# Performance work log

Hardware: AMD Instinct MI355X
Metric: run time of the kernel (lower is better)

The kernel has to match this reference:

```python
import jax, jax.numpy as jnp
import numpy as np

B = 1024
IN_H, IN_W = 128, 128
KH, KW = 10, 10
SH, SW = 5, 5
PH, PW = 2, 2
HP, WP = IN_H + 2 * PH, IN_W + 2 * PW          # padded dims: 132, 132
NKH = (IN_H - KH + 2 * PH) // SH + 1            # 25
NKW = (IN_W - KW + 2 * PW) // SW + 1            # 25
NK = NKH * NKW                                  # 625


def _build_weight_matrix(kernel_weights):
    """kernel_weights: [NK, KH, KW] -> sparse-structured dense [HP*WP, NK].
    Faithful to LocallyConnected2dV2._create_weight_matrix, vectorized."""
    i = jnp.arange(NK)
    start_i = (i // NKW) * SH                   # [NK]
    start_j = (i % NKW) * SW                    # [NK]
    # flat row index for each (kernel, k, l) tap in padded image
    rows = ((start_i[:, None, None] + jnp.arange(KH)[None, :, None]) * WP
            + start_j[:, None, None] + jnp.arange(KW)[None, None, :])  # [NK,KH,KW]
    rows = rows.reshape(NK, KH * KW)
    cols = i[:, None]                           # [NK,1] broadcasts over taps
    W = jnp.zeros((HP * WP, NK), dtype=kernel_weights.dtype)
    return W.at[rows, cols].set(kernel_weights.reshape(NK, KH * KW))


def setup_inputs() -> dict:
    key = jax.random.key(0)
    kx, kw, kb = jax.random.split(key, 3)
    x = jax.random.normal(kx, (B, IN_H, IN_W), dtype=jnp.float32)
    kernel_weights = jax.random.normal(kw, (NK, KH, KW), dtype=jnp.float32)
    W = _build_weight_matrix(kernel_weights)    # [HP*WP, NK]
    bias = jax.random.normal(kb, (NKH, NKW), dtype=jnp.float32)
    return {"x": x, "W": W, "bias": bias}


def reference(x, W, bias):
    # zero-pad spatial dims, flatten, dense GEMM against sparse-structured W
    xp = jnp.pad(x, ((0, 0), (PH, PH), (PW, PW)))          # [B,HP,WP]
    xf = xp.reshape(x.shape[0], HP * WP)                   # [B,HP*WP]
    out = xf @ W                                           # [B,NK]
    out = out.reshape(x.shape[0], NKH, NKW)
    return out + bias
```

## Files before the change

### kernel.cpp

```cpp
#include <hip/hip_runtime.h>

typedef _Float16 f16x2 __attribute__((ext_vector_type(2)));
typedef __fp16  fp16x2 __attribute__((ext_vector_type(2)));

constexpr int NKW  = 25, NK = 625;
constexpr int WPADR = 132;
constexpr int WPT   = 160;
constexpr int RST   = 35;
constexpr int IMG   = 8;
constexpr int NSLAB = 6;
constexpr int MAXR  = 30;

union U2H { unsigned int u; f16x2 h; fp16x2 p; };

__global__ void gather_wp(const float* __restrict__ W, _Float16* __restrict__ wgpT) {
    int t = blockIdx.x * 256 + threadIdx.x;
    if (t >= NK * WPT) return;
    int k = t / WPT, p = t % WPT;
    int di = p >> 4, s = p & 15;
    int ki = k / NKW, kj = k % NKW;
    int o = (5 * kj + 2) & 3;
    int j = s - o;
    float val = 0.f;
    if (j >= 0 && j < 10)
        val = W[(size_t)((ki * 5 + di) * WPADR + kj * 5 + j) * NK + k];
    wgpT[((size_t)(p >> 3) * NK + k) * 8 + (p & 7)] = (_Float16)val;
}

__device__ __forceinline__ float dot2acc(unsigned int a, unsigned int b, float c) {
    U2H ua, ub; ua.u = a; ub.u = b;
#if __has_builtin(__builtin_amdgcn_fdot2)
    return __builtin_amdgcn_fdot2(ua.h, ub.h, c, false);
#else
    return c + (float)ua.h.x * (float)ub.h.x + (float)ua.h.y * (float)ub.h.y;
#endif
}

template <bool USE_WG>
__global__ __launch_bounds__(256, 4)
void lc2d_pipe(const float* __restrict__ x, const _Float16* __restrict__ wgpT,
               const float* __restrict__ Wfull,
               const float* __restrict__ bias, float* __restrict__ out) {
    __shared__ uint2 xs[2][MAXR * RST];

    const int flat = blockIdx.x;
    const int xcd  = flat & 7;
    const int j_   = flat >> 3;
    const int grp  = xcd + 8 * (j_ & 15);
    const int slab = j_ >> 4;
    const int K0   = slab ? (4 * slab + 1) : 0;
    const int NKI  = slab ? 4 : 5;
    const int R    = 5 * NKI + 5;
    const int NOUT = NKI * NKW;
    const int row0 = 5 * K0 - 2;
    const int tid  = threadIdx.x;
    const int b0   = grp * IMG;

    const int lane = tid & 63;
    const int pairidx = (tid >> 6) * 32 + (lane & 31);
    const int half = (lane >> 5) & 1;
    const bool active = pairidx < NOUT;
    const int ki_l = pairidx / 25;
    const int kj   = pairidx - ki_l * 25;
    const int k    = (K0 + ki_l) * NKW + kj;
    const int di0  = half * 5;

    uint4 wq[10];
    float bval = 0.f;
    if (active) {
        if (USE_WG) {
            const uint4* wt4 = reinterpret_cast<const uint4*>(wgpT);
#pragma unroll
            for (int j = 0; j < 10; ++j) wq[j] = wt4[(size_t)(half * 10 + j) * NK + k];
        } else {
            const int o = (5 * kj + 2) & 3;
#pragma unroll
            for (int j = 0; j < 10; ++j) {
                const int di = di0 + (j >> 1), pb = (j & 1) * 8;
                unsigned int uu[4];
#pragma unroll
                for (int m = 0; m < 4; ++m) {
                    float f0 = 0.f, f1 = 0.f;
                    const int j0 = pb + 2 * m - o, j1 = pb + 2 * m + 1 - o;
                    const size_t rowb = (size_t)(((K0 + ki_l) * 5 + di) * WPADR + kj * 5);
                    if (j0 >= 0 && j0 < 10) f0 = Wfull[(rowb + j0) * NK + k];
                    if (j1 >= 0 && j1 < 10) f1 = Wfull[(rowb + j1) * NK + k];
                    U2H u; u.p = __builtin_amdgcn_cvt_pkrtz(f0, f1);
                    uu[m] = u.u;
                }
                wq[j] = make_uint4(uu[0], uu[1], uu[2], uu[3]);
            }
        }
        if (half == 0) bval = bias[k];
    }

    for (int i = tid; i < 4 * R; i += 256)
        xs[i & 1][(i >> 2) * RST + ((i >> 1) & 1) * 33] = make_uint2(0u, 0u);

    auto stage_load = [&](int img, float4* tmp) {
        const float* xb = x + ((size_t)(b0 + img) << 14);
#pragma unroll
        for (int t = 0; t < 4; ++t) {
            const int i = tid + t * 256;
            tmp[t] = make_float4(0.f, 0.f, 0.f, 0.f);
            if (i < R * 32) {
                const int idx = i >> 5, q = i & 31;
                const int r = row0 + idx;
                if (r >= 0 && r < 128)
                    tmp[t] = *reinterpret_cast<const float4*>(xb + (r << 7) + (q << 2));
            }
        }
    };
    auto stage_write = [&](int buf, const float4* tmp) {
#pragma unroll
        for (int t = 0; t < 4; ++t) {
            const int i = tid + t * 256;
            if (i < R * 32) {
                const int idx = i >> 5, q = (i & 31) + 1;
                U2H u0, u1;
                u0.p = __builtin_amdgcn_cvt_pkrtz(tmp[t].x, tmp[t].y);
                u1.p = __builtin_amdgcn_cvt_pkrtz(tmp[t].z, tmp[t].w);
                xs[buf][idx * RST + q] = make_uint2(u0.u, u1.u);
            }
        }
    };

    float4 tmpA[4], tmpB[4];
    stage_load(0, tmpA);
    stage_write(0, tmpA);
    stage_load(1, tmpB);
    __syncthreads();

    for (int i = 0; i < IMG; ++i) {
        if (i + 2 < IMG) stage_load(i + 2, (i & 1) ? tmpB : tmpA);

        float acc0 = 0.f, acc1 = 0.f;
        if (active) {
            const uint2* base = xs[i & 1] + (5 * ki_l + di0) * RST + ((5 * kj + 2) >> 2);
#pragma unroll
            for (int d = 0; d < 5; ++d) {
                const uint2* rowp = base + d * RST;
                const uint2 a0 = rowp[0], a1 = rowp[1], a2 = rowp[2], a3 = rowp[3];
                const uint4 wA = wq[2 * d], wB = wq[2 * d + 1];
                acc0 = dot2acc(a0.x, wA.x, acc0);
                acc1 = dot2acc(a0.y, wA.y, acc1);
                acc0 = dot2acc(a1.x, wA.z, acc0);
                acc1 = dot2acc(a1.y, wA.w, acc1);
                acc0 = dot2acc(a2.x, wB.x, acc0);
                acc1 = dot2acc(a2.y, wB.y, acc1);
                acc0 = dot2acc(a3.x, wB.z, acc0);
                acc1 = dot2acc(a3.y, wB.w, acc1);
            }
        }
        float acc = acc0 + acc1;
        float other = __shfl_xor(acc, 32, 64);
        if (active && half == 0)
            out[(size_t)(b0 + i) * NK + k] = acc + other + bval;

        if (i + 1 < IMG) stage_write((i + 1) & 1, (i & 1) ? tmpA : tmpB);
        __syncthreads();
    }
}

extern "C" void kernel_launch(void* const* d_in, const int* in_sizes, int n_in,
                              void* d_out, int out_size, void* d_ws, size_t ws_size,
                              hipStream_t stream) {
    const float* x    = (const float*)d_in[0];
    const float* W    = (const float*)d_in[1];
    const float* bias = (const float*)d_in[2];
    float* out = (float*)d_out;

    const dim3 grid(128 * NSLAB);
    if (ws_size >= (size_t)NK * WPT * sizeof(_Float16)) {
        _Float16* wgpT = (_Float16*)d_ws;
        gather_wp<<<(NK * WPT + 255) / 256, 256, 0, stream>>>(W, wgpT);
        lc2d_pipe<true><<<grid, 256, 0, stream>>>(x, wgpT, W, bias, out);
    } else {
        lc2d_pipe<false><<<grid, 256, 0, stream>>>(x, nullptr, W, bias, out);
    }
}
```

Baseline: 121.4 us.

## Restructure to one block per image with whole-image LDS tile and streamed weights

```diff
diff --git a/kernel.cpp b/kernel.cpp
--- a/kernel.cpp
+++ b/kernel.cpp
@@ -7,9 +7,8 @@
 constexpr int WPADR = 132;
 constexpr int WPT   = 160;
 constexpr int RST   = 35;
-constexpr int IMG   = 8;
-constexpr int NSLAB = 6;
-constexpr int MAXR  = 30;
+constexpr int RTOT  = 132;
+constexpr int NCHUNK = 5;
 
 union U2H { unsigned int u; f16x2 h; fp16x2 p; };
 
@@ -38,41 +37,56 @@
 
 template <bool USE_WG>
 __global__ __launch_bounds__(256, 4)
-void lc2d_pipe(const float* __restrict__ x, const _Float16* __restrict__ wgpT,
-               const float* __restrict__ Wfull,
-               const float* __restrict__ bias, float* __restrict__ out) {
-    __shared__ uint2 xs[2][MAXR * RST];
+void lc2d_img(const float* __restrict__ x, const _Float16* __restrict__ wgpT,
+              const float* __restrict__ Wfull,
+              const float* __restrict__ bias, float* __restrict__ out) {
+    __shared__ uint2 xs[RTOT * RST];
 
-    const int flat = blockIdx.x;
-    const int xcd  = flat & 7;
-    const int j_   = flat >> 3;
-    const int grp  = xcd + 8 * (j_ & 15);
-    const int slab = j_ >> 4;
-    const int K0   = slab ? (4 * slab + 1) : 0;
-    const int NKI  = slab ? 4 : 5;
-    const int R    = 5 * NKI + 5;
-    const int NOUT = NKI * NKW;
-    const int row0 = 5 * K0 - 2;
+    const int b    = blockIdx.x;
     const int tid  = threadIdx.x;
-    const int b0   = grp * IMG;
-
     const int lane = tid & 63;
-    const int pairidx = (tid >> 6) * 32 + (lane & 31);
-    const int half = (lane >> 5) & 1;
-    const bool active = pairidx < NOUT;
-    const int ki_l = pairidx / 25;
-    const int kj   = pairidx - ki_l * 25;
-    const int k    = (K0 + ki_l) * NKW + kj;
+    const int pairbase = (tid >> 6) * 32 + (lane & 31);
+    const int half = lane >> 5;
     const int di0  = half * 5;
 
-    uint4 wq[10];
-    float bval = 0.f;
-    if (active) {
-        if (USE_WG) {
+    const float* xb = x + ((size_t)b << 14);
+#pragma unroll 1
+    for (int bt = 0; bt < 3; ++bt) {
+        float4 tmp[6];
+#pragma unroll
+        for (int u = 0; u < 6; ++u) {
+            const int i = tid + (bt * 6 + u) * 256;
+            tmp[u] = make_float4(0.f, 0.f, 0.f, 0.f);
+            if (i < RTOT * 32) {
+                const int idx = i >> 5, q = i & 31, r = idx - 2;
+                if (r >= 0 && r < 128)
+                    tmp[u] = *reinterpret_cast<const float4*>(xb + (r << 7) + (q << 2));
+            }
+        }
+#pragma unroll
+        for (int u = 0; u < 6; ++u) {
+            const int i = tid + (bt * 6 + u) * 256;
+            if (i < RTOT * 32) {
+                const int idx = i >> 5, q = (i & 31) + 1;
+                U2H u0, u1;
+                u0.p = __builtin_amdgcn_cvt_pkrtz(tmp[u].x, tmp[u].y);
+                u1.p = __builtin_amdgcn_cvt_pkrtz(tmp[u].z, tmp[u].w);
+                xs[idx * RST + q] = make_uint2(u0.u, u1.u);
+            }
+        }
+    }
+    for (int i = tid; i < 2 * RTOT; i += 256)
+        xs[(i >> 1) * RST + (i & 1) * 33] = make_uint2(0u, 0u);
+
+    auto load_w = [&](int c, uint4* w, float& bv) {
+        const int pr = c * 128 + pairbase;
+        if (pr >= NK) return;
+        if constexpr (USE_WG) {
             const uint4* wt4 = reinterpret_cast<const uint4*>(wgpT);
 #pragma unroll
-            for (int j = 0; j < 10; ++j) wq[j] = wt4[(size_t)(half * 10 + j) * NK + k];
+            for (int j = 0; j < 10; ++j) w[j] = wt4[(size_t)(half * 10 + j) * NK + pr];
         } else {
+            const int ki = pr / 25, kj = pr - ki * 25;
             const int o = (5 * kj + 2) & 3;
 #pragma unroll
             for (int j = 0; j < 10; ++j) {
@@ -82,66 +96,29 @@
                 for (int m = 0; m < 4; ++m) {
                     float f0 = 0.f, f1 = 0.f;
                     const int j0 = pb + 2 * m - o, j1 = pb + 2 * m + 1 - o;
-                    const size_t rowb = (size_t)(((K0 + ki_l) * 5 + di) * WPADR + kj * 5);
-                    if (j0 >= 0 && j0 < 10) f0 = Wfull[(rowb + j0) * NK + k];
-                    if (j1 >= 0 && j1 < 10) f1 = Wfull[(rowb + j1) * NK + k];
+                    const size_t rowb = (size_t)((ki * 5 + di) * WPADR + kj * 5);
+                    if (j0 >= 0 && j0 < 10) f0 = Wfull[(rowb + j0) * NK + pr];
+                    if (j1 >= 0 && j1 < 10) f1 = Wfull[(rowb + j1) * NK + pr];
                     U2H u; u.p = __builtin_amdgcn_cvt_pkrtz(f0, f1);
                     uu[m] = u.u;
                 }
-                wq[j] = make_uint4(uu[0], uu[1], uu[2], uu[3]);
+                w[j] = make_uint4(uu[0], uu[1], uu[2], uu[3]);
             }
         }
-        if (half == 0) bval = bias[k];
-    }
-
-    for (int i = tid; i < 4 * R; i += 256)
-        xs[i & 1][(i >> 2) * RST + ((i >> 1) & 1) * 33] = make_uint2(0u, 0u);
-
-    auto stage_load = [&](int img, float4* tmp) {
-        const float* xb = x + ((size_t)(b0 + img) << 14);
-#pragma unroll
-        for (int t = 0; t < 4; ++t) {
-            const int i = tid + t * 256;
-            tmp[t] = make_float4(0.f, 0.f, 0.f, 0.f);
-            if (i < R * 32) {
-                const int idx = i >> 5, q = i & 31;
-                const int r = row0 + idx;
-                if (r >= 0 && r < 128)
-                    tmp[t] = *reinterpret_cast<const float4*>(xb + (r << 7) + (q << 2));
-            }
-        }
-    };
-    auto stage_write = [&](int buf, const float4* tmp) {
-#pragma unroll
-        for (int t = 0; t < 4; ++t) {
-            const int i = tid + t * 256;
-            if (i < R * 32) {
-                const int idx = i >> 5, q = (i & 31) + 1;
-                U2H u0, u1;
-                u0.p = __builtin_amdgcn_cvt_pkrtz(tmp[t].x, tmp[t].y);
-                u1.p = __builtin_amdgcn_cvt_pkrtz(tmp[t].z, tmp[t].w);
-                xs[buf][idx * RST + q] = make_uint2(u0.u, u1.u);
-            }
-        }
+        if (half == 0) bv = bias[pr];
     };
 
-    float4 tmpA[4], tmpB[4];
-    stage_load(0, tmpA);
-    stage_write(0, tmpA);
-    stage_load(1, tmpB);
-    __syncthreads();
-
-    for (int i = 0; i < IMG; ++i) {
-        if (i + 2 < IMG) stage_load(i + 2, (i & 1) ? tmpB : tmpA);
-
+    auto compute_chunk = [&](int c, const uint4* w, float bv) {
+        const int pr = c * 128 + pairbase;
         float acc0 = 0.f, acc1 = 0.f;
-        if (active) {
-            const uint2* base = xs[i & 1] + (5 * ki_l + di0) * RST + ((5 * kj + 2) >> 2);
+        if (pr < NK) {
+            const int ki = pr / 25, kj = pr - ki * 25;
+            const uint2* base = xs + (5 * ki + di0) * RST + ((5 * kj + 2) >> 2);
 #pragma unroll
             for (int d = 0; d < 5; ++d) {
                 const uint2* rowp = base + d * RST;
                 const uint2 a0 = rowp[0], a1 = rowp[1], a2 = rowp[2], a3 = rowp[3];
-                const uint4 wA = wq[2 * d], wB = wq[2 * d + 1];
+                const uint4 wA = w[2 * d], wB = w[2 * d + 1];
                 acc0 = dot2acc(a0.x, wA.x, acc0);
                 acc1 = dot2acc(a0.y, wA.y, acc1);
                 acc0 = dot2acc(a1.x, wA.z, acc0);
@@ -154,12 +131,20 @@
         }
         float acc = acc0 + acc1;
         float other = __shfl_xor(acc, 32, 64);
-        if (active && half == 0)
-            out[(size_t)(b0 + i) * NK + k] = acc + other + bval;
+        if (pr < NK && half == 0)
+            out[(size_t)b * NK + pr] = acc + other + bv;
+    };
 
-        if (i + 1 < IMG) stage_write((i + 1) & 1, (i & 1) ? tmpA : tmpB);
-        __syncthreads();
-    }
+    uint4 wA[10], wB[10];
+    float bA = 0.f, bB = 0.f;
+    load_w(0, wA, bA);
+    load_w(1, wB, bB);
+    __syncthreads();
+    compute_chunk(0, wA, bA); load_w(2, wA, bA);
+    compute_chunk(1, wB, bB); load_w(3, wB, bB);
+    compute_chunk(2, wA, bA); load_w(4, wA, bA);
+    compute_chunk(3, wB, bB);
+    compute_chunk(4, wA, bA);
 }
 
 extern "C" void kernel_launch(void* const* d_in, const int* in_sizes, int n_in,
@@ -170,12 +155,12 @@
     const float* bias = (const float*)d_in[2];
     float* out = (float*)d_out;
 
-    const dim3 grid(128 * NSLAB);
+    const dim3 grid(1024);
     if (ws_size >= (size_t)NK * WPT * sizeof(_Float16)) {
         _Float16* wgpT = (_Float16*)d_ws;
         gather_wp<<<(NK * WPT + 255) / 256, 256, 0, stream>>>(W, wgpT);
-        lc2d_pipe<true><<<grid, 256, 0, stream>>>(x, wgpT, W, bias, out);
+        lc2d_img<true><<<grid, 256, 0, stream>>>(x, wgpT, W, bias, out);
     } else {
-        lc2d_pipe<false><<<grid, 256, 0, stream>>>(x, nullptr, W, bias, out);
+        lc2d_img<false><<<grid, 256, 0, stream>>>(x, nullptr, W, bias, out);
     }
 }
```

Result: slower. 126.7 us (+4.4%).

## Assign one image per block and iterate over row bands with per-band weight reload

Applied to the files above, without the earlier changes.

```diff
diff --git a/kernel.cpp b/kernel.cpp
--- a/kernel.cpp
+++ b/kernel.cpp
@@ -7,9 +7,9 @@
 constexpr int WPADR = 132;
 constexpr int WPT   = 160;
 constexpr int RST   = 35;
-constexpr int IMG   = 8;
-constexpr int NSLAB = 6;
-constexpr int MAXR  = 30;
+constexpr int BROWS = 30;
+constexpr int BITEM = BROWS * 32;
+constexpr int NBAND = 5;
 
 union U2H { unsigned int u; f16x2 h; fp16x2 p; };
 
@@ -38,41 +38,61 @@
 
 template <bool USE_WG>
 __global__ __launch_bounds__(256, 4)
-void lc2d_pipe(const float* __restrict__ x, const _Float16* __restrict__ wgpT,
+void lc2d_band(const float* __restrict__ x, const _Float16* __restrict__ wgpT,
                const float* __restrict__ Wfull,
                const float* __restrict__ bias, float* __restrict__ out) {
-    __shared__ uint2 xs[2][MAXR * RST];
+    __shared__ uint2 xs[2][BROWS * RST];
 
-    const int flat = blockIdx.x;
-    const int xcd  = flat & 7;
-    const int j_   = flat >> 3;
-    const int grp  = xcd + 8 * (j_ & 15);
-    const int slab = j_ >> 4;
-    const int K0   = slab ? (4 * slab + 1) : 0;
-    const int NKI  = slab ? 4 : 5;
-    const int R    = 5 * NKI + 5;
-    const int NOUT = NKI * NKW;
-    const int row0 = 5 * K0 - 2;
+    const int b    = blockIdx.x;
     const int tid  = threadIdx.x;
-    const int b0   = grp * IMG;
-
     const int lane = tid & 63;
     const int pairidx = (tid >> 6) * 32 + (lane & 31);
-    const int half = (lane >> 5) & 1;
-    const bool active = pairidx < NOUT;
+    const int half = lane >> 5;
+    const int di0  = half * 5;
+    const bool active = pairidx < 125;
     const int ki_l = pairidx / 25;
     const int kj   = pairidx - ki_l * 25;
-    const int k    = (K0 + ki_l) * NKW + kj;
-    const int di0  = half * 5;
+    const float* xb = x + ((size_t)b << 14);
+
+    float4 tmp[4];
+    auto band_load = [&](int t) {
+        const int r0 = 25 * t - 2;
+#pragma unroll
+        for (int u = 0; u < 4; ++u) {
+            const int i = tid + u * 256;
+            tmp[u] = make_float4(0.f, 0.f, 0.f, 0.f);
+            if (i < BITEM) {
+                const int r = r0 + (i >> 5), q = i & 31;
+                if (r >= 0 && r < 128)
+                    tmp[u] = *reinterpret_cast<const float4*>(xb + (r << 7) + (q << 2));
+            }
+        }
+    };
+    auto band_write = [&](int buf) {
+#pragma unroll
+        for (int u = 0; u < 4; ++u) {
+            const int i = tid + u * 256;
+            if (i < BITEM) {
+                const int idx = i >> 5, q = (i & 31) + 1;
+                U2H u0h, u1h;
+                u0h.p = __builtin_amdgcn_cvt_pkrtz(tmp[u].x, tmp[u].y);
+                u1h.p = __builtin_amdgcn_cvt_pkrtz(tmp[u].z, tmp[u].w);
+                xs[buf][idx * RST + q] = make_uint2(u0h.u, u1h.u);
+            }
+        }
+    };
 
     uint4 wq[10];
-    float bval = 0.f;
-    if (active) {
-        if (USE_WG) {
+    float bv = 0.f;
+    auto load_w = [&](int t) {
+        if (!active) return;
+        const int k = 125 * t + pairidx;
+        if constexpr (USE_WG) {
             const uint4* wt4 = reinterpret_cast<const uint4*>(wgpT);
 #pragma unroll
             for (int j = 0; j < 10; ++j) wq[j] = wt4[(size_t)(half * 10 + j) * NK + k];
         } else {
+            const int ki = 5 * t + ki_l;
             const int o = (5 * kj + 2) & 3;
 #pragma unroll
             for (int j = 0; j < 10; ++j) {
@@ -82,7 +102,7 @@
                 for (int m = 0; m < 4; ++m) {
                     float f0 = 0.f, f1 = 0.f;
                     const int j0 = pb + 2 * m - o, j1 = pb + 2 * m + 1 - o;
-                    const size_t rowb = (size_t)(((K0 + ki_l) * 5 + di) * WPADR + kj * 5);
+                    const size_t rowb = (size_t)((ki * 5 + di) * WPADR + kj * 5);
                     if (j0 >= 0 && j0 < 10) f0 = Wfull[(rowb + j0) * NK + k];
                     if (j1 >= 0 && j1 < 10) f1 = Wfull[(rowb + j1) * NK + k];
                     U2H u; u.p = __builtin_amdgcn_cvt_pkrtz(f0, f1);
@@ -91,52 +111,13 @@
                 wq[j] = make_uint4(uu[0], uu[1], uu[2], uu[3]);
             }
         }
-        if (half == 0) bval = bias[k];
-    }
-
-    for (int i = tid; i < 4 * R; i += 256)
-        xs[i & 1][(i >> 2) * RST + ((i >> 1) & 1) * 33] = make_uint2(0u, 0u);
-
-    auto stage_load = [&](int img, float4* tmp) {
-        const float* xb = x + ((size_t)(b0 + img) << 14);
-#pragma unroll
-        for (int t = 0; t < 4; ++t) {
-            const int i = tid + t * 256;
-            tmp[t] = make_float4(0.f, 0.f, 0.f, 0.f);
-            if (i < R * 32) {
-                const int idx = i >> 5, q = i & 31;
-                const int r = row0 + idx;
-                if (r >= 0 && r < 128)
-                    tmp[t] = *reinterpret_cast<const float4*>(xb + (r << 7) + (q << 2));
-            }
-        }
-    };
-    auto stage_write = [&](int buf, const float4* tmp) {
-#pragma unroll
-        for (int t = 0; t < 4; ++t) {
-            const int i = tid + t * 256;
-            if (i < R * 32) {
-                const int idx = i >> 5, q = (i & 31) + 1;
-                U2H u0, u1;
-                u0.p = __builtin_amdgcn_cvt_pkrtz(tmp[t].x, tmp[t].y);
-                u1.p = __builtin_amdgcn_cvt_pkrtz(tmp[t].z, tmp[t].w);
-                xs[buf][idx * RST + q] = make_uint2(u0.u, u1.u);
-            }
-        }
+        if (half == 0) bv = bias[k];
     };
 
-    float4 tmpA[4], tmpB[4];
-    stage_load(0, tmpA);
-    stage_write(0, tmpA);
-    stage_load(1, tmpB);
-    __syncthreads();
-
-    for (int i = 0; i < IMG; ++i) {
-        if (i + 2 < IMG) stage_load(i + 2, (i & 1) ? tmpB : tmpA);
-
+    auto compute = [&](int t, int buf) {
         float acc0 = 0.f, acc1 = 0.f;
         if (active) {
-            const uint2* base = xs[i & 1] + (5 * ki_l + di0) * RST + ((5 * kj + 2) >> 2);
+            const uint2* base = xs[buf] + (5 * ki_l + di0) * RST + ((5 * kj + 2) >> 2);
 #pragma unroll
             for (int d = 0; d < 5; ++d) {
                 const uint2* rowp = base + d * RST;
@@ -155,10 +136,26 @@
         float acc = acc0 + acc1;
         float other = __shfl_xor(acc, 32, 64);
         if (active && half == 0)
-            out[(size_t)(b0 + i) * NK + k] = acc + other + bval;
+            out[(size_t)b * NK + 125 * t + pairidx] = acc + other + bv;
+    };
 
-        if (i + 1 < IMG) stage_write((i + 1) & 1, (i & 1) ? tmpA : tmpB);
-        __syncthreads();
+    for (int i = tid; i < 4 * BROWS; i += 256)
+        xs[i & 1][(i >> 2) * RST + ((i >> 1) & 1) * 33] = make_uint2(0u, 0u);
+
+    band_load(0);
+    band_write(0);
+    load_w(0);
+    __syncthreads();
+
+#pragma unroll
+    for (int t = 0; t < NBAND; ++t) {
+        if (t + 1 < NBAND) band_load(t + 1);
+        compute(t, t & 1);
+        if (t + 1 < NBAND) {
+            load_w(t + 1);
+            band_write((t + 1) & 1);
+            __syncthreads();
+        }
     }
 }
 
@@ -170,12 +167,12 @@
     const float* bias = (const float*)d_in[2];
     float* out = (float*)d_out;
 
-    const dim3 grid(128 * NSLAB);
+    const dim3 grid(1024);
     if (ws_size >= (size_t)NK * WPT * sizeof(_Float16)) {
         _Float16* wgpT = (_Float16*)d_ws;
         gather_wp<<<(NK * WPT + 255) / 256, 256, 0, stream>>>(W, wgpT);
-        lc2d_pipe<true><<<grid, 256, 0, stream>>>(x, wgpT, W, bias, out);
+        lc2d_band<true><<<grid, 256, 0, stream>>>(x, wgpT, W, bias, out);
     } else {
-        lc2d_pipe<false><<<grid, 256, 0, stream>>>(x, nullptr, W, bias, out);
+        lc2d_band<false><<<grid, 256, 0, stream>>>(x, nullptr, W, bias, out);
     }
 }
```

New measurement: 127.7 us. +5.3%, slower.
